# Optimization experiments

Hardware: AMD Instinct MI355X
Metric: run time of the kernel (lower is better)

## Reference

```python
import jax, jax.numpy as jnp
import numpy as np

PADDING_L = 15  # init arg padding_l

def setup_inputs() -> dict:
    key = jax.random.key(0)
    k1, k2 = jax.random.split(key)
    T, B, C = 2048, 2, 1024
    H, K = 16, 31
    x = jax.random.normal(k1, (T, B, C), dtype=jnp.float32)
    # xavier-uniform-ish init for (H, 1, K)
    limit = float(np.sqrt(6.0 / (1 + K)))
    weight = jax.random.uniform(k2, (H, 1, K), dtype=jnp.float32, minval=-limit, maxval=limit)
    return {"x": x, "weight": weight}


def reference(x, weight):
    T, B, C = x.shape
    H, _, K = weight.shape
    R = C // H
    P = PADDING_L
    # softmax-normalized per-head kernel weights (weight_softmax path)
    w = jax.nn.softmax(weight.reshape(H, K), axis=1)  # (H, K)

    # --- output: depthwise 'same' conv, out[t] = sum_k w[k] * x[t - P + k] ---
    kern = jnp.repeat(w, R, axis=0)[:, None, :]       # (C, 1, K)
    xb = jnp.transpose(x, (1, 2, 0))                   # (B, C, T)
    out = jax.lax.conv_general_dilated(
        xb, kern, window_strides=(1,), padding=[(P, K - 1 - P)],
        dimension_numbers=("NCH", "OIH", "NCH"), feature_group_count=C)
    output = jnp.transpose(out, (2, 0, 1))             # (T, B, C)

    # --- weight_expanded: banded Toeplitz matrix, returned by the module ---
    t = jnp.arange(T)
    off = t[None, :] - t[:, None] + P                  # (T, T), band offset
    valid = (off >= 0) & (off < K)
    band = jnp.where(valid, w[:, jnp.clip(off, 0, K - 1)], 0.0)  # (H, T, T)
    weight_expanded = jnp.broadcast_to(band[None], (B, H, T, T)).reshape(B * H, T, T)

    return output, weight_expanded
```

## Files before the change

kernel.cpp:

```cpp
#include <hip/hip_runtime.h>

#define T_DIM 2048
#define B_DIM 2
#define C_DIM 1024
#define H_DIM 16
#define K_DIM 31
#define P_PAD 15
#define BC    (B_DIM * C_DIM)
#define TT    32

#define CONV_BLOCKS 512
#define XBLOCKS     2048
#define GRID_BLKS   (CONV_BLOCKS + XBLOCKS)
#define E1 32u
#define E2 56u

typedef float v4f __attribute__((ext_vector_type(4)));

__global__ __launch_bounds__(256) void k_fused(const float* __restrict__ x,
                                               const float* __restrict__ w,
                                               float* __restrict__ out,
                                               float* __restrict__ we) {
    __shared__ float lw[H_DIM * K_DIM];
    const int tid = threadIdx.x;

    if (tid < H_DIM) {
        float v[K_DIM];
        float m = -1e30f;
#pragma unroll
        for (int k = 0; k < K_DIM; ++k) { v[k] = w[tid * K_DIM + k]; m = fmaxf(m, v[k]); }
        float s = 0.f;
#pragma unroll
        for (int k = 0; k < K_DIM; ++k) { v[k] = expf(v[k] - m); s += v[k]; }
        float inv = 1.f / s;
#pragma unroll
        for (int k = 0; k < K_DIM; ++k) lw[tid * K_DIM + k] = v[k] * inv;
    }
    __syncthreads();

    const int bid = blockIdx.x;
    unsigned ubase, ucnt;

    if (bid < CONV_BLOCKS) {
        const int colBase = (bid & 7) * 256;
        const int t0      = (bid >> 3) * TT;
        const int col     = colBase + tid;
        const int h       = (col & (C_DIM - 1)) >> 6;

        float wr[K_DIM];
#pragma unroll
        for (int k = 0; k < K_DIM; ++k) wr[k] = lw[h * K_DIM + k];

        float xv[TT + K_DIM - 1];
#pragma unroll
        for (int r = 0; r < TT + K_DIM - 1; ++r) {
            int t = t0 - P_PAD + r;
            xv[r] = (t >= 0 && t < T_DIM) ? x[t * BC + col] : 0.f;
        }
#pragma unroll
        for (int i = 0; i < TT; ++i) {
            float acc = 0.f;
#pragma unroll
            for (int k = 0; k < K_DIM; ++k) acc = fmaf(wr[k], xv[i + k], acc);
            out[(t0 + i) * BC + col] = acc;
        }
        ubase = (unsigned)bid * E1;  ucnt = E1;
    } else {
        ubase = CONV_BLOCKS * E1 + (unsigned)(bid - CONV_BLOCKS) * E2;  ucnt = E2;
    }

    v4f* we4 = (v4f*)we;
#pragma unroll 4
    for (unsigned u = 0; u < ucnt; ++u) {
        const unsigned f   = (ubase + u) * 256u + (unsigned)tid;
        const unsigned bh  = f >> 20;
        const unsigned rem = f & 0xFFFFFu;
        const unsigned i   = rem >> 9;
        const int      j4  = (int)((rem & 511u) << 2);
        const int      d   = j4 - (int)i + P_PAD;

        v4f v = (v4f)0.f;
        if (d > -4 && d < K_DIM) {
            const float* wrow = lw + (bh & (H_DIM - 1)) * K_DIM;
            v.x = (d     >= 0 && d     < K_DIM) ? wrow[d]     : 0.f;
            v.y = (d + 1 >= 0 && d + 1 < K_DIM) ? wrow[d + 1] : 0.f;
            v.z = (d + 2 >= 0 && d + 2 < K_DIM) ? wrow[d + 2] : 0.f;
            v.w = (d + 3 >= 0 && d + 3 < K_DIM) ? wrow[d + 3] : 0.f;
        }
        __builtin_nontemporal_store(v, we4 + f);
    }
}

extern "C" void kernel_launch(void* const* d_in, const int* in_sizes, int n_in,
                              void* d_out, int out_size, void* d_ws, size_t ws_size,
                              hipStream_t stream) {
    const float* x = (const float*)d_in[0];
    const float* w = (const float*)d_in[1];
    float* out = (float*)d_out;
    float* we  = out + (size_t)T_DIM * B_DIM * C_DIM;

    k_fused<<<GRID_BLKS, 256, 0, stream>>>(x, w, out, we);
}
```

Baseline: 116.1 us.

## Zero Toeplitz output with memset and write only the band from the kernel

Instead of having every thread compute and nontemporally store the full dense Toeplitz matrix, the launch first zeroes the whole weight_expanded buffer with hipMemsetAsync. The kernel's band blocks then write only a 256-byte window around each row's diagonal band. This hands the bulk zero-fill to the driver's memset path. In exchange it adds a separate memset operation and a second write pass over the band region, and the conv work no longer overlaps with the zero-fill.

```diff
diff --git a/kernel.cpp b/kernel.cpp
--- a/kernel.cpp
+++ b/kernel.cpp
@@ -10,17 +10,16 @@
 #define TT    32
 
 #define CONV_BLOCKS 512
-#define XBLOCKS     2048
-#define GRID_BLKS   (CONV_BLOCKS + XBLOCKS)
-#define E1 32u
-#define E2 56u
+#define BAND_BLOCKS 256
+#define GRID_BLKS   (CONV_BLOCKS + BAND_BLOCKS)
+#define ROW_BYTES   8192
 
 typedef float v4f __attribute__((ext_vector_type(4)));
 
-__global__ __launch_bounds__(256) void k_fused(const float* __restrict__ x,
-                                               const float* __restrict__ w,
-                                               float* __restrict__ out,
-                                               float* __restrict__ we) {
+__global__ __launch_bounds__(256) void k_conv_band(const float* __restrict__ x,
+                                                   const float* __restrict__ w,
+                                                   float* __restrict__ out,
+                                                   float* __restrict__ we) {
     __shared__ float lw[H_DIM * K_DIM];
     const int tid = threadIdx.x;
 
@@ -39,7 +38,6 @@
     __syncthreads();
 
     const int bid = blockIdx.x;
-    unsigned ubase, ucnt;
 
     if (bid < CONV_BLOCKS) {
         const int colBase = (bid & 7) * 256;
@@ -64,30 +62,33 @@
             for (int k = 0; k < K_DIM; ++k) acc = fmaf(wr[k], xv[i + k], acc);
             out[(t0 + i) * BC + col] = acc;
         }
-        ubase = (unsigned)bid * E1;  ucnt = E1;
     } else {
-        ubase = CONV_BLOCKS * E1 + (unsigned)(bid - CONV_BLOCKS) * E2;  ucnt = E2;
-    }
+        const int rowBase = (bid - CONV_BLOCKS) * 256;
+        const int sub = tid >> 4;
+        const int l16 = tid & 15;
 
-    v4f* we4 = (v4f*)we;
 #pragma unroll 4
-    for (unsigned u = 0; u < ucnt; ++u) {
-        const unsigned f   = (ubase + u) * 256u + (unsigned)tid;
-        const unsigned bh  = f >> 20;
-        const unsigned rem = f & 0xFFFFFu;
-        const unsigned i   = rem >> 9;
-        const int      j4  = (int)((rem & 511u) << 2);
-        const int      d   = j4 - (int)i + P_PAD;
+        for (int step = 0; step < 16; ++step) {
+            const int r  = rowBase + step * 16 + sub;
+            const int bh = r >> 11;
+            const int i  = r & (T_DIM - 1);
+            const float* wrow = lw + (bh & (H_DIM - 1)) * K_DIM;
 
-        v4f v = (v4f)0.f;
-        if (d > -4 && d < K_DIM) {
-            const float* wrow = lw + (bh & (H_DIM - 1)) * K_DIM;
-            v.x = (d     >= 0 && d     < K_DIM) ? wrow[d]     : 0.f;
-            v.y = (d + 1 >= 0 && d + 1 < K_DIM) ? wrow[d + 1] : 0.f;
-            v.z = (d + 2 >= 0 && d + 2 < K_DIM) ? wrow[d + 2] : 0.f;
-            v.w = (d + 3 >= 0 && d + 3 < K_DIM) ? wrow[d + 3] : 0.f;
+            int s = 4 * i - 60;
+            if (s < 0) s = 0;
+            s &= ~127;
+            const int byte0 = s + l16 * 16;
+            if (byte0 < ROW_BYTES) {
+                const int j0 = byte0 >> 2;
+                v4f v;
+#pragma unroll
+                for (int e = 0; e < 4; ++e) {
+                    const int d = j0 + e - i + P_PAD;
+                    v[e] = (d >= 0 && d < K_DIM) ? wrow[d] : 0.f;
+                }
+                *(v4f*)((char*)we + ((size_t)r << 13) + byte0) = v;
+            }
         }
-        __builtin_nontemporal_store(v, we4 + f);
     }
 }
 
@@ -99,5 +100,7 @@
     float* out = (float*)d_out;
     float* we  = out + (size_t)T_DIM * B_DIM * C_DIM;
 
-    k_fused<<<GRID_BLKS, 256, 0, stream>>>(x, w, out, we);
+    hipMemsetAsync(we, 0, 32ull * T_DIM * T_DIM * sizeof(float), stream);
+
+    k_conv_band<<<GRID_BLKS, 256, 0, stream>>>(x, w, out, we);
 }
```

After: 107.2 us. 7.7% less time.
